# Kernel tuning notes

Hardware: AMD Instinct MI355X
Metric: run time of the kernel (lower is better)

Reference implementation:

```python
import jax, jax.numpy as jnp
import numpy as np

N = 500_000   # nodes
E = 1_250_000 # edges
CIN, H = 2, 64
EPS = 1e-5


def setup_inputs() -> dict:
    key = jax.random.key(0)
    ks = jax.random.split(key, 16)
    def w(k, i, o):
        return jax.random.normal(k, (i, o), jnp.float32) / np.sqrt(i)
    return {
        "x": jax.random.normal(ks[0], (N, CIN), jnp.float32),
        "edge_index": jax.random.randint(ks[1], (2, E), 0, N, jnp.int64),
        # SAGEConv layer 1 (lin_l on aggregated neighbors has bias, lin_r on root has none)
        "W1l": w(ks[2], CIN, H), "b1": jnp.zeros((H,), jnp.float32), "W1r": w(ks[3], CIN, H),
        "g1": jnp.ones((H,), jnp.float32), "be1": jnp.zeros((H,), jnp.float32),
        # SAGEConv layer 2
        "W2l": w(ks[4], H, H), "b2": jnp.zeros((H,), jnp.float32), "W2r": w(ks[5], H, H),
        "g2": jnp.ones((H,), jnp.float32), "be2": jnp.zeros((H,), jnp.float32),
        # SAGEConv layer 3 -> 1 channel
        "W3l": w(ks[6], H, 1), "b3": jnp.zeros((1,), jnp.float32), "W3r": w(ks[7], H, 1),
    }


def _sage(x, src, dst, Wl, b, Wr, n):
    # mean aggregation of source-node features into target nodes
    agg = jax.ops.segment_sum(x[src], dst, num_segments=n)           # [N, d_in]
    deg = jax.ops.segment_sum(jnp.ones((src.shape[0], 1), x.dtype), dst, num_segments=n)
    agg = agg / jnp.maximum(deg, 1.0)
    return agg @ Wl + b + x @ Wr


def _bn(x, g, be):
    m = jnp.mean(x, axis=0)
    v = jnp.var(x, axis=0)  # biased var, as torch BN uses for normalization
    return (x - m) * jax.lax.rsqrt(v + EPS) * g + be


def reference(x, edge_index, W1l, b1, W1r, g1, be1, W2l, b2, W2r, g2, be2, W3l, b3, W3r):
    src, dst = edge_index[0], edge_index[1]
    n = x.shape[0]
    x1 = jax.nn.relu(_bn(_sage(x, src, dst, W1l, b1, W1r, n), g1, be1))
    x2 = jax.nn.relu(_bn(_sage(x1, src, dst, W2l, b2, W2r, n), g2, be2))
    x2 = x2 + x1  # residual
    x3 = _sage(x2, src, dst, W3l, b3, W3r, n)
    return x3.reshape(-1)
```

## Files before the change

kernel.cpp:

```cpp
#include <hip/hip_runtime.h>

#define EPS 1e-5f

typedef __attribute__((ext_vector_type(8))) short bf16x8;
typedef __attribute__((ext_vector_type(4))) float f32x4;

__device__ __forceinline__ unsigned short f2bf(float f) {
    unsigned u = __float_as_uint(f);
    u += 0x7fffu + ((u >> 16) & 1u);
    return (unsigned short)(u >> 16);
}
__device__ __forceinline__ float bf2f(unsigned short s) {
    return __uint_as_float(((unsigned)s) << 16);
}


__global__ void k_detect(const int* __restrict__ ei, int* __restrict__ flag) {
    if (blockIdx.x == 0 && threadIdx.x == 0) {
        int is64 = 1;
        for (int k = 0; k < 16; ++k) is64 &= (ei[2 * k + 1] == 0) ? 1 : 0;
        *flag = is64;
    }
}

__global__ void k_hist(const int* __restrict__ ei, const int* __restrict__ flag,
                       int E, int* __restrict__ cnt) {
    int e = blockIdx.x * blockDim.x + threadIdx.x;
    if (e >= E) return;
    int d = (*flag) ? (int)((const long long*)ei)[E + e] : ei[E + e];
    atomicAdd(&cnt[d], 1);
}

__device__ __forceinline__ int block_incl_scan(int v, int tid, int* total) {
    __shared__ int wsum[4];
    __shared__ int tot;
#pragma unroll
    for (int o = 1; o < 64; o <<= 1) {
        int u = __shfl_up(v, o, 64);
        if ((tid & 63) >= o) v += u;
    }
    if ((tid & 63) == 63) wsum[tid >> 6] = v;
    __syncthreads();
    int w = tid >> 6, add = 0;
    if (w > 0) add += wsum[0];
    if (w > 1) add += wsum[1];
    if (w > 2) add += wsum[2];
    v += add;
    if (tid == 255) tot = v;
    __syncthreads();
    *total = tot;
    __syncthreads();
    return v;
}

__global__ __launch_bounds__(256) void k_scanA(const int* __restrict__ cnt, int n,
                                               int* __restrict__ bsums) {
    int tid = threadIdx.x;
    int idx = blockIdx.x * 1024 + tid * 4;
    int s = 0;
#pragma unroll
    for (int k = 0; k < 4; ++k) { int i = idx + k; if (i < n) s += cnt[i]; }
#pragma unroll
    for (int o = 32; o > 0; o >>= 1) s += __shfl_xor(s, o, 64);
    __shared__ int ws[4];
    if ((tid & 63) == 0) ws[tid >> 6] = s;
    __syncthreads();
    if (tid == 0) bsums[blockIdx.x] = ws[0] + ws[1] + ws[2] + ws[3];
}

__global__ __launch_bounds__(256) void k_scanB(int* __restrict__ bsums, int nb,
                                               int* __restrict__ rowptr, int N) {
    int tid = threadIdx.x;
    __shared__ int sh_carry;
    if (tid == 0) sh_carry = 0;
    __syncthreads();
    int niter = (nb + 255) / 256;
    for (int it = 0; it < niter; ++it) {
        int i = it * 256 + tid;
        int v = (i < nb) ? bsums[i] : 0;
        int tot;
        int inc = block_incl_scan(v, tid, &tot);
        int carry = sh_carry;
        if (i < nb) bsums[i] = carry + inc - v;
        __syncthreads();
        if (tid == 0) sh_carry = carry + tot;
        __syncthreads();
    }
    if (tid == 0) rowptr[N] = sh_carry;
}

__global__ __launch_bounds__(256) void k_scanC(int* __restrict__ cnt_rowptr, int n,
                                               const int* __restrict__ bsums,
                                               int* __restrict__ cursor) {
    int tid = threadIdx.x;
    int idx = blockIdx.x * 1024 + tid * 4;
    int v[4]; int s = 0;
#pragma unroll
    for (int k = 0; k < 4; ++k) { int i = idx + k; v[k] = (i < n) ? cnt_rowptr[i] : 0; s += v[k]; }
    int tot;
    int inc = block_incl_scan(s, tid, &tot);
    int off = bsums[blockIdx.x] + inc - s;
#pragma unroll
    for (int k = 0; k < 4; ++k) {
        int i = idx + k;
        if (i < n) { cnt_rowptr[i] = off; cursor[i] = off; off += v[k]; }
    }
}

__global__ void k_fill_range(const int* __restrict__ ei, const int* __restrict__ flag,
                             int E, int* __restrict__ cursor, int* __restrict__ csr,
                             int lo, int hi) {
    int e = blockIdx.x * blockDim.x + threadIdx.x;
    if (e >= E) return;
    int f = *flag;
    int d = f ? (int)((const long long*)ei)[E + e] : ei[E + e];
    if (d < lo || d >= hi) return;
    int s = f ? (int)((const long long*)ei)[e] : ei[e];
    int pos = atomicAdd(&cursor[d], 1);
    csr[pos] = s;
}

__global__ __launch_bounds__(256) void k_gather1m(
    const float* __restrict__ x, const int* __restrict__ rowptr,
    const int* __restrict__ csr, float* __restrict__ agg1,
    float* __restrict__ pmom, int n) {
    int tid = threadIdx.x;
    int i = blockIdx.x * 256 + tid;
    float m[14];
#pragma unroll
    for (int k = 0; k < 14; ++k) m[k] = 0.f;
    if (i < n) {
        int r0 = rowptr[i], r1 = rowptr[i + 1];
        float s0 = 0.f, s1 = 0.f;
        int j = r0;
        for (; j + 3 < r1; j += 4) {
            float2 v0 = ((const float2*)x)[csr[j]];
            float2 v1 = ((const float2*)x)[csr[j + 1]];
            float2 v2 = ((const float2*)x)[csr[j + 2]];
            float2 v3 = ((const float2*)x)[csr[j + 3]];
            s0 += v0.x + v1.x + v2.x + v3.x;
            s1 += v0.y + v1.y + v2.y + v3.y;
        }
        for (; j < r1; ++j) {
            float2 v = ((const float2*)x)[csr[j]];
            s0 += v.x; s1 += v.y;
        }
        float inv = 1.f / fmaxf((float)(r1 - r0), 1.f);
        float ax = s0 * inv, ay = s1 * inv;
        agg1[2 * i] = ax;
        agg1[2 * i + 1] = ay;
        float2 xv = ((const float2*)x)[i];
        m[0] = ax;        m[1] = ay;        m[2] = xv.x;      m[3] = xv.y;
        m[4] = ax * ax;   m[5] = ax * ay;   m[6] = ax * xv.x; m[7] = ax * xv.y;
        m[8] = ay * ay;   m[9] = ay * xv.x; m[10] = ay * xv.y;
        m[11] = xv.x * xv.x; m[12] = xv.x * xv.y; m[13] = xv.y * xv.y;
    }
#pragma unroll
    for (int k = 0; k < 14; ++k) {
#pragma unroll
        for (int o = 32; o > 0; o >>= 1) m[k] += __shfl_xor(m[k], o, 64);
    }
    __shared__ float red[4][14];
    int w = tid >> 6;
    if ((tid & 63) == 0) {
#pragma unroll
        for (int k = 0; k < 14; ++k) red[w][k] = m[k];
    }
    __syncthreads();
    if (tid < 14)
        pmom[(size_t)tid * gridDim.x + blockIdx.x] =
            red[0][tid] + red[1][tid] + red[2][tid] + red[3][tid];
}

__global__ __launch_bounds__(256) void k_bnfold1(
    const float* __restrict__ pmom, int gn,
    const float* __restrict__ W1l, const float* __restrict__ b1,
    const float* __restrict__ W1r,
    const float* __restrict__ g1, const float* __restrict__ be1,
    float* __restrict__ fold, float invN) {
    int tid = threadIdx.x;
    __shared__ float smom[14];
    __shared__ float ws[4];
    for (int k = 0; k < 14; ++k) {
        float s = 0.f;
        for (int idx = tid; idx < gn; idx += 256) s += pmom[(size_t)k * gn + idx];
#pragma unroll
        for (int o = 32; o > 0; o >>= 1) s += __shfl_xor(s, o, 64);
        if ((tid & 63) == 0) ws[tid >> 6] = s;
        __syncthreads();
        if (tid == 0) smom[k] = ws[0] + ws[1] + ws[2] + ws[3];
        __syncthreads();
    }
    if (tid < 64) {
        int c = tid;
        float w0 = W1l[c], w1 = W1l[64 + c], w2 = W1r[c], w3 = W1r[64 + c], w4 = b1[c];
        float lin = (smom[0] * w0 + smom[1] * w1 + smom[2] * w2 + smom[3] * w3) * invN;
        float mean = lin + w4;
        float q = smom[4] * w0 * w0 + smom[8] * w1 * w1 + smom[11] * w2 * w2 + smom[13] * w3 * w3
                + 2.f * (smom[5] * w0 * w1 + smom[6] * w0 * w2 + smom[7] * w0 * w3
                       + smom[9] * w1 * w2 + smom[10] * w1 * w3 + smom[12] * w2 * w3);
        float Eh2 = q * invN + 2.f * w4 * lin + w4 * w4;
        float var = Eh2 - mean * mean;
        float al = g1[c] * rsqrtf(var + EPS);
        float be = be1[c] - mean * al;
        fold[c]       = al * w0;
        fold[64 + c]  = al * w1;
        fold[128 + c] = al * w2;
        fold[192 + c] = al * w3;
        fold[256 + c] = al * w4 + be;
    }
}

__global__ __launch_bounds__(256) void k_sredfin(
    const float* __restrict__ pstats, int nb,
    const float* __restrict__ g, const float* __restrict__ be,
    float* __restrict__ coef, float invN) {
    int c = blockIdx.x, tid = threadIdx.x;
    float s = 0.f, q = 0.f;
    for (int i = tid; i < nb; i += 256) {
        s += pstats[(size_t)c * nb + i];
        q += pstats[(size_t)(64 + c) * nb + i];
    }
#pragma unroll
    for (int o = 32; o > 0; o >>= 1) {
        s += __shfl_xor(s, o, 64);
        q += __shfl_xor(q, o, 64);
    }
    __shared__ float ws[4], wq[4];
    if ((tid & 63) == 0) { ws[tid >> 6] = s; wq[tid >> 6] = q; }
    __syncthreads();
    if (tid == 0) {
        float S = ws[0] + ws[1] + ws[2] + ws[3];
        float Q = wq[0] + wq[1] + wq[2] + wq[3];
        float m = S * invN;
        float var = Q * invN - m * m;
        int o = (c & 3) * 16 + (c >> 2);
        float a = g[o] * rsqrtf(var + EPS);
        coef[c] = a;
        coef[64 + c] = be[o] - m * a;
    }
}

__global__ __launch_bounds__(256) void k_dense_pre(
    const float* __restrict__ agg1, const float* __restrict__ xin,
    const float* __restrict__ fold,
    const float* __restrict__ W2l, const float* __restrict__ b2,
    const float* __restrict__ W2r,
    const float* __restrict__ W3l, const float* __restrict__ W3r,
    unsigned short* __restrict__ y, unsigned short* __restrict__ z,
    float* __restrict__ t1, float* __restrict__ v1, int n) {
    __shared__ unsigned short lds_w[16 * 64 * 8];
    int tid = threadIdx.x, w = tid >> 6, l = tid & 63, ln = l & 15, kg = l >> 4;

    for (int idx = tid; idx < 4096; idx += 256) {
        int k = idx >> 6, c = idx & 63;
        int lane = ((k >> 3) & 3) * 16 + (c & 15);
        int fbase = ((k >> 5) * 4 + (c >> 4)) * 64 + lane;
        lds_w[fbase * 8 + (k & 7)] = f2bf(W2l[idx]);
        lds_w[(8 * 64 + fbase) * 8 + (k & 7)] = f2bf(W2r[idx]);
    }
    __syncthreads();

    float bb[4];
#pragma unroll
    for (int cs = 0; cs < 4; ++cs) bb[cs] = b2[cs * 16 + ln];

    float F0[16], F1[16], F2[16], F3[16], F4[16];
#pragma unroll
    for (int j = 0; j < 8; ++j) {
        int c = kg * 8 + j;
        F0[j] = fold[c];       F1[j] = fold[64 + c];  F2[j] = fold[128 + c];
        F3[j] = fold[192 + c]; F4[j] = fold[256 + c];
        c += 32;
        F0[8 + j] = fold[c];       F1[8 + j] = fold[64 + c];  F2[8 + j] = fold[128 + c];
        F3[8 + j] = fold[192 + c]; F4[8 + j] = fold[256 + c];
    }
    bf16x8 b3a, b3b;
#pragma unroll
    for (int j = 0; j < 8; ++j) {
        float va = (ln == 0) ? W3l[kg * 8 + j] : ((ln == 1) ? W3r[kg * 8 + j] : 0.f);
        float vb = (ln == 0) ? W3l[32 + kg * 8 + j] : ((ln == 1) ? W3r[32 + kg * 8 + j] : 0.f);
        b3a[j] = (short)f2bf(va);
        b3b[j] = (short)f2bf(vb);
    }

    const bf16x8* wfrag = (const bf16x8*)lds_w;
    int nt = (n + 15) >> 4;
    int stride = gridDim.x * 4;

#define LOADH(T, A)                                                          \
    {                                                                        \
        int row_ = ((T) << 4) + ln;                                          \
        int rr_ = (row_ < n) ? row_ : (n - 1);                               \
        A##a = ((const float2*)agg1)[rr_];                                   \
        A##x = ((const float2*)xin)[rr_];                                    \
    }

#define PROCESSH(T, A)                                                       \
    {                                                                        \
        bf16x8 u0_, u1_;                                                     \
        _Pragma("unroll")                                                    \
        for (int j = 0; j < 8; ++j) {                                        \
            float h0_ = fmaf(A##a.x, F0[j], fmaf(A##a.y, F1[j],              \
                        fmaf(A##x.x, F2[j], fmaf(A##x.y, F3[j], F4[j]))));   \
            float h1_ = fmaf(A##a.x, F0[8 + j], fmaf(A##a.y, F1[8 + j],      \
                        fmaf(A##x.x, F2[8 + j], fmaf(A##x.y, F3[8 + j], F4[8 + j])))); \
            u0_[j] = (short)f2bf(fmaxf(0.f, h0_));                           \
            u1_[j] = (short)f2bf(fmaxf(0.f, h1_));                           \
        }                                                                    \
        f32x4 ya_[4], za_[4], a3_;                                           \
        _Pragma("unroll")                                                    \
        for (int cs = 0; cs < 4; ++cs) {                                     \
            ya_[cs] = (f32x4){0.f, 0.f, 0.f, 0.f};                           \
            za_[cs] = (f32x4){0.f, 0.f, 0.f, 0.f};                           \
        }                                                                    \
        a3_ = (f32x4){0.f, 0.f, 0.f, 0.f};                                   \
        _Pragma("unroll")                                                    \
        for (int cs = 0; cs < 4; ++cs) {                                     \
            ya_[cs] = __builtin_amdgcn_mfma_f32_16x16x32_bf16(u0_, wfrag[(0 * 4 + cs) * 64 + l], ya_[cs], 0, 0, 0);  \
            ya_[cs] = __builtin_amdgcn_mfma_f32_16x16x32_bf16(u1_, wfrag[(1 * 4 + cs) * 64 + l], ya_[cs], 0, 0, 0);  \
            za_[cs] = __builtin_amdgcn_mfma_f32_16x16x32_bf16(u0_, wfrag[(8 + cs) * 64 + l], za_[cs], 0, 0, 0);      \
            za_[cs] = __builtin_amdgcn_mfma_f32_16x16x32_bf16(u1_, wfrag[(12 + cs) * 64 + l], za_[cs], 0, 0, 0);     \
        }                                                                    \
        a3_ = __builtin_amdgcn_mfma_f32_16x16x32_bf16(u0_, b3a, a3_, 0, 0, 0); \
        a3_ = __builtin_amdgcn_mfma_f32_16x16x32_bf16(u1_, b3b, a3_, 0, 0, 0); \
        int base_ = (T) << 4;                                                \
        _Pragma("unroll")                                                    \
        for (int r = 0; r < 4; ++r) {                                        \
            int row_ = base_ + kg * 4 + r;                                   \
            if (row_ < n) {                                                  \
                ushort4 yv_, zv_;                                            \
                yv_.x = f2bf(ya_[0][r]); yv_.y = f2bf(ya_[1][r]);            \
                yv_.z = f2bf(ya_[2][r]); yv_.w = f2bf(ya_[3][r]);            \
                zv_.x = f2bf(za_[0][r] + bb[0]); zv_.y = f2bf(za_[1][r] + bb[1]); \
                zv_.z = f2bf(za_[2][r] + bb[2]); zv_.w = f2bf(za_[3][r] + bb[3]); \
                *(ushort4*)(y + (size_t)row_ * 64 + ln * 4) = yv_;           \
                *(ushort4*)(z + (size_t)row_ * 64 + ln * 4) = zv_;           \
            }                                                                \
        }                                                                    \
        if (ln < 2) {                                                        \
            float* d3_ = (ln == 0) ? t1 : v1;                                \
            _Pragma("unroll")                                                \
            for (int r = 0; r < 4; ++r) {                                    \
                int row_ = base_ + kg * 4 + r;                               \
                if (row_ < n) d3_[row_] = a3_[r];                            \
            }                                                                \
        }                                                                    \
    }

    float2 Pa, Px, Qa, Qx;
    int t = blockIdx.x * 4 + w;
    if (t < nt) {
        LOADH(t, P);
        while (t < nt) {
            int t1_ = t + stride;
            if (t1_ < nt) LOADH(t1_, Q);
            PROCESSH(t, P);
            int t2_ = t1_ + stride;
            if (t2_ < nt) LOADH(t2_, P);
            if (t1_ < nt) PROCESSH(t1_, Q);
            t = t2_;
        }
    }
#undef LOADH
#undef PROCESSH
}

__global__ __launch_bounds__(256) void k_gather2b(
    const unsigned short* __restrict__ y, const int* __restrict__ rowptr,
    const int* __restrict__ csr, unsigned short* zh2,
    float* __restrict__ pstats, int n) {
    int tid = threadIdx.x;
    int lg = tid & 7;
    int gid0 = blockIdx.x * 32 + (tid >> 3);
    int gstep = gridDim.x * 32;
    float ls[8] = {0.f, 0.f, 0.f, 0.f, 0.f, 0.f, 0.f, 0.f};
    float lq[8] = {0.f, 0.f, 0.f, 0.f, 0.f, 0.f, 0.f, 0.f};

    for (int i = gid0; i < n; i += gstep) {
        bf16x8 z8 = *(const bf16x8*)(zh2 + (size_t)i * 64 + lg * 8);
        int r0 = rowptr[i], r1 = rowptr[i + 1];
        float s[8] = {0.f, 0.f, 0.f, 0.f, 0.f, 0.f, 0.f, 0.f};
        int j = r0;
        for (; j + 1 < r1; j += 2) {
            int a = csr[j], b = csr[j + 1];
            bf16x8 va = *(const bf16x8*)(y + (size_t)a * 64 + lg * 8);
            bf16x8 vb = *(const bf16x8*)(y + (size_t)b * 64 + lg * 8);
#pragma unroll
            for (int k = 0; k < 8; ++k)
                s[k] += bf2f((unsigned short)va[k]) + bf2f((unsigned short)vb[k]);
        }
        if (j < r1) {
            bf16x8 va = *(const bf16x8*)(y + (size_t)csr[j] * 64 + lg * 8);
#pragma unroll
            for (int k = 0; k < 8; ++k) s[k] += bf2f((unsigned short)va[k]);
        }
        float inv = 1.f / fmaxf((float)(r1 - r0), 1.f);
        bf16x8 hb;
#pragma unroll
        for (int k = 0; k < 8; ++k) {
            float h = fmaf(s[k], inv, bf2f((unsigned short)z8[k]));
            unsigned short b = f2bf(h);
            hb[k] = (short)b;
            float hf = bf2f(b);
            ls[k] += hf; lq[k] += hf * hf;
        }
        *(bf16x8*)(zh2 + (size_t)i * 64 + lg * 8) = hb;
    }

#pragma unroll
    for (int k = 0; k < 8; ++k) {
        ls[k] += __shfl_xor(ls[k], 8, 64);
        ls[k] += __shfl_xor(ls[k], 16, 64);
        ls[k] += __shfl_xor(ls[k], 32, 64);
        lq[k] += __shfl_xor(lq[k], 8, 64);
        lq[k] += __shfl_xor(lq[k], 16, 64);
        lq[k] += __shfl_xor(lq[k], 32, 64);
    }
    __shared__ float red[2][4][64];
    int w = tid >> 6;
    if ((tid & 63) < 8) {
#pragma unroll
        for (int k = 0; k < 8; ++k) {
            red[0][w][lg * 8 + k] = ls[k];
            red[1][w][lg * 8 + k] = lq[k];
        }
    }
    __syncthreads();
    if (tid < 128) {
        int c = tid & 63;
        int half = tid >> 6;
        float v = red[half][0][c] + red[half][1][c] + red[half][2][c] + red[half][3][c];
        pstats[(size_t)tid * gridDim.x + blockIdx.x] = v;
    }
}

__global__ __launch_bounds__(256) void k_finalize(
    const unsigned short* __restrict__ h2b,
    const float* __restrict__ t1, const float* __restrict__ v1,
    const float* __restrict__ coef2,
    const float* __restrict__ W3l, const float* __restrict__ W3r,
    float* __restrict__ tb, float* __restrict__ vb, int n) {
    int tid = threadIdx.x, w = tid >> 6, l = tid & 63, ln = l & 15, kg = l >> 4;

    float c2a[16], c2b[16];
#pragma unroll
    for (int j = 0; j < 8; ++j) {
        c2a[j]     = coef2[kg * 8 + j];       c2b[j]     = coef2[64 + kg * 8 + j];
        c2a[8 + j] = coef2[32 + kg * 8 + j];  c2b[8 + j] = coef2[96 + kg * 8 + j];
    }
    bf16x8 b3a, b3b;
#pragma unroll
    for (int j = 0; j < 8; ++j) {
        int k0 = kg * 8 + j;
        int k1 = 32 + kg * 8 + j;
        int o0 = (k0 & 3) * 16 + (k0 >> 2);
        int o1 = (k1 & 3) * 16 + (k1 >> 2);
        float va = (ln == 0) ? W3l[o0] : ((ln == 1) ? W3r[o0] : 0.f);
        float vb = (ln == 0) ? W3l[o1] : ((ln == 1) ? W3r[o1] : 0.f);
        b3a[j] = (short)f2bf(va);
        b3b[j] = (short)f2bf(vb);
    }

    int t = blockIdx.x * 4 + w;
    int nt = (n + 15) >> 4;
    if (t >= nt) return;
    int i0 = t << 4;
    int row = i0 + ln;
    int rr = (row < n) ? row : (n - 1);
    const unsigned short* hr = h2b + (size_t)rr * 64 + kg * 8;
    bf16x8 r0 = *(const bf16x8*)hr;
    bf16x8 r1 = *(const bf16x8*)(hr + 32);
    bf16x8 u0, u1;
#pragma unroll
    for (int j = 0; j < 8; ++j) {
        float f0 = bf2f((unsigned short)r0[j]);
        float f1 = bf2f((unsigned short)r1[j]);
        u0[j] = (short)f2bf(fmaxf(0.f, fmaf(f0, c2a[j], c2b[j])));
        u1[j] = (short)f2bf(fmaxf(0.f, fmaf(f1, c2a[8 + j], c2b[8 + j])));
    }
    f32x4 acc = (f32x4){0.f, 0.f, 0.f, 0.f};
    acc = __builtin_amdgcn_mfma_f32_16x16x32_bf16(u0, b3a, acc, 0, 0, 0);
    acc = __builtin_amdgcn_mfma_f32_16x16x32_bf16(u1, b3b, acc, 0, 0, 0);
    if (ln < 2) {
        float* d = (ln == 0) ? tb : vb;
        const float* s1 = (ln == 0) ? t1 : v1;
#pragma unroll
        for (int r = 0; r < 4; ++r) {
            int orow = i0 + kg * 4 + r;
            if (orow < n) d[orow] = acc[r] + s1[orow];
        }
    }
}

__global__ void k_gather3(const float* __restrict__ tb, const float* __restrict__ vb,
                          const int* __restrict__ rowptr, const int* __restrict__ csr,
                          const float* __restrict__ b3, float* __restrict__ out, int n) {
    int i = blockIdx.x * blockDim.x + threadIdx.x;
    if (i >= n) return;
    int r0 = rowptr[i], r1 = rowptr[i + 1];
    float s = 0.f;
    int j = r0;
    for (; j + 3 < r1; j += 4)
        s += tb[csr[j]] + tb[csr[j + 1]] + tb[csr[j + 2]] + tb[csr[j + 3]];
    for (; j < r1; ++j) s += tb[csr[j]];
    float inv = 1.f / fmaxf((float)(r1 - r0), 1.f);
    out[i] = fmaf(s, inv, b3[0] + vb[i]);
}

extern "C" void kernel_launch(void* const* d_in, const int* in_sizes, int n_in,
                              void* d_out, int out_size, void* d_ws, size_t ws_size,
                              hipStream_t stream) {
    const float* x   = (const float*)d_in[0];
    const int*   ei  = (const int*)d_in[1];
    const float* W1l = (const float*)d_in[2];
    const float* b1  = (const float*)d_in[3];
    const float* W1r = (const float*)d_in[4];
    const float* g1  = (const float*)d_in[5];
    const float* be1 = (const float*)d_in[6];
    const float* W2l = (const float*)d_in[7];
    const float* b2  = (const float*)d_in[8];
    const float* W2r = (const float*)d_in[9];
    const float* g2  = (const float*)d_in[10];
    const float* be2 = (const float*)d_in[11];
    const float* W3l = (const float*)d_in[12];
    const float* b3  = (const float*)d_in[13];
    const float* W3r = (const float*)d_in[14];

    int N = in_sizes[0] / 2;
    int E = in_sizes[1] / 2;

    float* ws   = (float*)d_ws;
    size_t nn   = (size_t)N;
    unsigned short* y   = (unsigned short*)ws;
    unsigned short* zh2 = (unsigned short*)(ws + 32 * nn);
    float* R     = ws + 64 * nn;
    int*   cursor = (int*)R;
    float* agg1   = R;
    float* tb     = R;
    float* vb     = R + nn;
    float* t1     = ws + 66 * nn;
    float* v1     = ws + 67 * nn;
    int*   rowptr = (int*)(ws + 68 * nn);
    int*   csr    = rowptr + (N + 1);
    int*   bsums  = csr + E;
    float* pstats = (float*)(bsums + 2048);
    float* pmom   = pstats + 128 * 2048;
    float* coef2  = pmom + 14 * 2048;
    float* fold   = coef2 + 128;
    int*   flag   = (int*)(fold + 320);

    hipMemsetAsync(rowptr, 0, (size_t)(N + 1) * sizeof(int), stream);

    k_detect<<<1, 1, 0, stream>>>(ei, flag);

    int ge = (E + 255) / 256;
    int gn = (N + 255) / 256;
    int nb = (N + 1023) / 1024;
    k_hist<<<ge, 256, 0, stream>>>(ei, flag, E, rowptr);
    k_scanA<<<nb, 256, 0, stream>>>(rowptr, N, bsums);
    k_scanB<<<1, 256, 0, stream>>>(bsums, nb, rowptr, N);
    k_scanC<<<nb, 256, 0, stream>>>(rowptr, N, bsums, cursor);
    {
        const int NPASS = 4;
        int span = (N + NPASS - 1) / NPASS;
        for (int p = 0; p < NPASS; ++p) {
            int lo = p * span;
            int hi = min(N, lo + span);
            k_fill_range<<<ge, 256, 0, stream>>>(ei, flag, E, cursor, csr, lo, hi);
        }
    }

    k_gather1m<<<gn, 256, 0, stream>>>(x, rowptr, csr, agg1, pmom, N);
    k_bnfold1<<<1, 256, 0, stream>>>(pmom, gn, W1l, b1, W1r, g1, be1, fold,
                                     1.0f / (float)N);

    k_dense_pre<<<2048, 256, 0, stream>>>(agg1, x, fold, W2l, b2, W2r, W3l, W3r,
                                          y, zh2, t1, v1, N);

    k_gather2b<<<2048, 256, 0, stream>>>(y, rowptr, csr, zh2, pstats, N);
    k_sredfin<<<64, 256, 0, stream>>>(pstats, 2048, g2, be2, coef2, 1.0f / (float)N);

    int nt = (N + 15) / 16;
    k_finalize<<<(nt + 3) / 4, 256, 0, stream>>>(zh2, t1, v1, coef2,
                                                 W3l, W3r, tb, vb, N);
    k_gather3<<<gn, 256, 0, stream>>>(tb, vb, rowptr, csr, b3, (float*)d_out, N);
}
```

Before: 350.3 us.

## Convert edge indices to int32 once and merge range-partitioned CSR build passes

Adds a conversion kernel that narrows the int64 edge index into compact int32 src/dst arrays. The histogram and CSR fill kernels then read these smaller arrays instead of re-reading 64-bit data on every pass. The four separate fill launches collapse into one launch whose block index selects the destination range. The histogram is also split into two destination ranges to localise atomics. This cuts repeated wide reads and launch overhead, at the cost of an extra conversion pass and extra workspace.

```diff
diff --git a/kernel.cpp b/kernel.cpp
--- a/kernel.cpp
+++ b/kernel.cpp
@@ -23,11 +23,27 @@
     }
 }
 
-__global__ void k_hist(const int* __restrict__ ei, const int* __restrict__ flag,
-                       int E, int* __restrict__ cnt) {
+__global__ void k_cvt(const int* __restrict__ ei, const int* __restrict__ flag,
+                      int E, int* __restrict__ d32, int* __restrict__ s32) {
     int e = blockIdx.x * blockDim.x + threadIdx.x;
     if (e >= E) return;
-    int d = (*flag) ? (int)((const long long*)ei)[E + e] : ei[E + e];
+    if (*flag) {
+        s32[e] = (int)((const long long*)ei)[e];
+        d32[e] = (int)((const long long*)ei)[E + e];
+    } else {
+        s32[e] = ei[e];
+        d32[e] = ei[E + e];
+    }
+}
+
+__global__ void k_hist2(const int* __restrict__ d32, int E, int ge,
+                        int* __restrict__ cnt, int span) {
+    int p = blockIdx.x / ge;
+    int e = (blockIdx.x - p * ge) * blockDim.x + threadIdx.x;
+    if (e >= E) return;
+    int d = d32[e];
+    int lo = p * span;
+    if (d < lo || d >= lo + span) return;
     atomicAdd(&cnt[d], 1);
 }
 
@@ -107,17 +123,17 @@
     }
 }
 
-__global__ void k_fill_range(const int* __restrict__ ei, const int* __restrict__ flag,
-                             int E, int* __restrict__ cursor, int* __restrict__ csr,
-                             int lo, int hi) {
-    int e = blockIdx.x * blockDim.x + threadIdx.x;
+__global__ void k_fill4(const int* __restrict__ d32, const int* __restrict__ s32,
+                        int E, int ge, int* __restrict__ cursor,
+                        int* __restrict__ csr, int span) {
+    int p = blockIdx.x / ge;
+    int e = (blockIdx.x - p * ge) * blockDim.x + threadIdx.x;
     if (e >= E) return;
-    int f = *flag;
-    int d = f ? (int)((const long long*)ei)[E + e] : ei[E + e];
-    if (d < lo || d >= hi) return;
-    int s = f ? (int)((const long long*)ei)[e] : ei[e];
+    int d = d32[e];
+    int lo = p * span;
+    if (d < lo || d >= lo + span) return;
     int pos = atomicAdd(&cursor[d], 1);
-    csr[pos] = s;
+    csr[pos] = s32[e];
 }
 
 __global__ __launch_bounds__(256) void k_gather1m(
@@ -543,7 +559,9 @@
     float* v1     = ws + 67 * nn;
     int*   rowptr = (int*)(ws + 68 * nn);
     int*   csr    = rowptr + (N + 1);
-    int*   bsums  = csr + E;
+    int*   d32    = csr + E;
+    int*   s32    = d32 + E;
+    int*   bsums  = s32 + E;
     float* pstats = (float*)(bsums + 2048);
     float* pmom   = pstats + 128 * 2048;
     float* coef2  = pmom + 14 * 2048;
@@ -557,18 +575,19 @@
     int ge = (E + 255) / 256;
     int gn = (N + 255) / 256;
     int nb = (N + 1023) / 1024;
-    k_hist<<<ge, 256, 0, stream>>>(ei, flag, E, rowptr);
+
+    k_cvt<<<ge, 256, 0, stream>>>(ei, flag, E, d32, s32);
+
+    {
+        int span = (N + 1) / 2;
+        k_hist2<<<2 * ge, 256, 0, stream>>>(d32, E, ge, rowptr, span);
+    }
     k_scanA<<<nb, 256, 0, stream>>>(rowptr, N, bsums);
     k_scanB<<<1, 256, 0, stream>>>(bsums, nb, rowptr, N);
     k_scanC<<<nb, 256, 0, stream>>>(rowptr, N, bsums, cursor);
     {
-        const int NPASS = 4;
-        int span = (N + NPASS - 1) / NPASS;
-        for (int p = 0; p < NPASS; ++p) {
-            int lo = p * span;
-            int hi = min(N, lo + span);
-            k_fill_range<<<ge, 256, 0, stream>>>(ei, flag, E, cursor, csr, lo, hi);
-        }
+        int span = (N + 3) / 4;
+        k_fill4<<<4 * ge, 256, 0, stream>>>(d32, s32, E, ge, cursor, csr, span);
     }
 
     k_gather1m<<<gn, 256, 0, stream>>>(x, rowptr, csr, agg1, pmom, N);
```

Result: no change. 347.7 us (-0.7%).
